# Performance work log

Measured on AMD Instinct MI355X. Metric: run time of the kernel, lower is better.

Reference implementation:

```python
import jax, jax.numpy as jnp
import numpy as np

N_USERS = 40000
N_ITEMS = 20000
NNZ = 1_000_000
D = 64
N_LAYERS = 3
EPS = 1e-8
PRUNING = 0.0  # forward default: pruning=0.0 -> get_sim_adj branch, threshold is a no-op


def setup_inputs() -> dict:
    key = jax.random.key(0)
    k1, k2, k3 = jax.random.split(key, 3)
    # unique-ish sorted edge codes -> coalesced COO order (sorted by (u, i))
    codes = jnp.sort(jax.random.randint(k3, (NNZ,), 0, N_USERS * N_ITEMS, dtype=jnp.int32))
    u_idx = codes // N_ITEMS
    i_idx = codes % N_ITEMS
    # xavier_uniform bound = sqrt(6/(fan_in+fan_out))
    b_u = float(np.sqrt(6.0 / (N_ITEMS + D)))
    b_i = float(np.sqrt(6.0 / (N_USERS + D)))
    user_linear = jax.random.uniform(k1, (N_ITEMS, D), jnp.float32, -b_u, b_u)
    item_linear = jax.random.uniform(k2, (N_USERS, D), jnp.float32, -b_i, b_i)
    return {"user_linear": user_linear, "item_linear": item_linear,
            "u_idx": u_idx, "i_idx": i_idx}


def reference(user_linear, item_linear, u_idx, i_idx):
    seg = jax.ops.segment_sum
    N = N_USERS + N_ITEMS
    # get_all_user_embedding: inter @ user_linear  -> [n_users, D]
    user_emb = seg(user_linear[i_idx], u_idx, num_segments=N_USERS)
    # get_all_item_embedding: inter.T @ item_linear -> [n_items, D]
    item_emb = seg(item_linear[u_idx], i_idx, num_segments=N_ITEMS)

    # sp_cos_sim: per-edge cosine similarity (chunked loop in torch == one vectorized gather)
    u_n = user_emb / jnp.maximum(jnp.linalg.norm(user_emb, axis=1, keepdims=True), EPS)
    i_n = item_emb / jnp.maximum(jnp.linalg.norm(item_emb, axis=1, keepdims=True), EPS)
    sims = jnp.sum(u_n[u_idx] * i_n[i_idx], axis=1)  # [nnz]
    # torch builds the sim sparse tensor with requires_grad=False -> detached
    sims = jax.lax.stop_gradient(sims)

    # inter2adj: values = [sims sorted by (u,i); sims sorted by (i,u)]
    sim_value = (sims + 1.0) * 0.5
    sim_value = jnp.where(sim_value < PRUNING, 0.0, sim_value) if PRUNING > 0 else sim_value
    perm = jnp.argsort(i_idx.astype(jnp.int32) * N_USERS + u_idx)  # (i,u) coalesce order
    rows = jnp.concatenate([u_idx, i_idx[perm] + N_USERS])          # [2*nnz]
    cols = jnp.concatenate([i_idx + N_USERS, u_idx[perm]])
    vals = jnp.concatenate([sim_value, sim_value[perm]])

    # row-normalize: D^-1 * A  (get_sim_adj)
    diags = seg(vals, rows, num_segments=N) + 1e-7
    vals = vals * (1.0 / diags)[rows]

    # LightGCN-style propagation
    all_emb = jnp.concatenate([user_emb, item_emb], axis=0)  # [N, D]
    embs = [all_emb]
    for _ in range(N_LAYERS):
        all_emb = seg(all_emb[cols] * vals[:, None], rows, num_segments=N)
        embs.append(all_emb)
    out = jnp.mean(jnp.stack(embs, axis=1), axis=1)  # [N, D]
    return out[:N_USERS], out[N_USERS:]
```

## Files before the change

kernel.cpp:

```cpp
#include <hip/hip_runtime.h>
#include <hip/hip_fp16.h>

#define N_USERS 40000
#define N_ITEMS 20000
#define N_TOTAL (N_USERS + N_ITEMS)
#define D 64
#define G_BKT ((N_ITEMS + 63) >> 6)
#define PAD 16

union H8 { uint4 u; __half h[8]; };

#define ZA (N_ITEMS * D / 8)
#define ZB (N_USERS * D / 8)
#define ZC (N_USERS + 1)
#define ZD ((G_BKT + 1) * PAD)
#define ZTOT (ZA + ZB + ZC + ZD)

__global__ void setup_kernel(const float* __restrict__ ul, const float* __restrict__ il,
                             const int* __restrict__ u_idx,
                             __half* __restrict__ ulH, __half* __restrict__ ilH,
                             int* __restrict__ pu, int* __restrict__ bcnt, int nnz) {
    int t = blockIdx.x * blockDim.x + threadIdx.x;
    if (t < ZA) {
        const float4* s = (const float4*)(ul + (size_t)t * 8);
        float4 a = s[0], b = s[1];
        H8 o;
        o.h[0] = __float2half(a.x); o.h[1] = __float2half(a.y);
        o.h[2] = __float2half(a.z); o.h[3] = __float2half(a.w);
        o.h[4] = __float2half(b.x); o.h[5] = __float2half(b.y);
        o.h[6] = __float2half(b.z); o.h[7] = __float2half(b.w);
        ((uint4*)ulH)[t] = o.u;
    } else if (t < ZA + ZB) {
        int q = t - ZA;
        const float4* s = (const float4*)(il + (size_t)q * 8);
        float4 a = s[0], b = s[1];
        H8 o;
        o.h[0] = __float2half(a.x); o.h[1] = __float2half(a.y);
        o.h[2] = __float2half(a.z); o.h[3] = __float2half(a.w);
        o.h[4] = __float2half(b.x); o.h[5] = __float2half(b.y);
        o.h[6] = __float2half(b.z); o.h[7] = __float2half(b.w);
        ((uint4*)ilH)[q] = o.u;
    } else if (t < ZA + ZB + ZC) {
        int u = t - (ZA + ZB);
        int lo = 0, hi = nnz;
        while (lo < hi) { int mid = (lo + hi) >> 1; if (u_idx[mid] < u) lo = mid + 1; else hi = mid; }
        pu[u] = lo;
    } else if (t < ZTOT) {
        bcnt[t - (ZA + ZB + ZC)] = 0;
    }
}


__global__ void bcount_kernel(const int* __restrict__ i_idx, int* __restrict__ bcnt, int nnz) {
    __shared__ int lc[G_BKT];
    for (int t = threadIdx.x; t < G_BKT; t += blockDim.x) lc[t] = 0;
    __syncthreads();
    int stride = gridDim.x * blockDim.x;
    for (int e = blockIdx.x * blockDim.x + threadIdx.x; e < nnz; e += stride)
        atomicAdd(&lc[__builtin_nontemporal_load(i_idx + e) >> 6], 1);
    __syncthreads();
    for (int t = threadIdx.x; t < G_BKT; t += blockDim.x)
        if (lc[t]) atomicAdd(bcnt + t * PAD, lc[t]);
}

__global__ void bscan_kernel(const int* __restrict__ bcnt, int* __restrict__ bbase,
                             int* __restrict__ bcur, int* __restrict__ pi, int nnz) {
    if (threadIdx.x == 0 && blockIdx.x == 0) {
        int run = 0;
        for (int g = 0; g < G_BKT; ++g) {
            bbase[g * PAD] = run;
            bcur[g * PAD] = run;
            run += bcnt[g * PAD];
        }
        bbase[G_BKT * PAD] = run;
        pi[N_ITEMS] = run;
    }
}

__global__ void p1_kernel(const int* __restrict__ i_idx, const int* __restrict__ u_idx,
                          int* __restrict__ bcur, int2* __restrict__ tmp, int nnz) {
    const int E = 8;
    __shared__ int lc[G_BKT];
    __shared__ int gb[G_BKT];
    for (int t = threadIdx.x; t < G_BKT; t += blockDim.x) lc[t] = 0;
    __syncthreads();
    int base_e = blockIdx.x * blockDim.x * E;
    int myb[E], myr[E]; int2 myv[E];
    #pragma unroll
    for (int j = 0; j < E; ++j) {
        int e = base_e + j * blockDim.x + threadIdx.x;
        myb[j] = -1;
        if (e < nnz) {
            int i = __builtin_nontemporal_load(i_idx + e);
            int u = __builtin_nontemporal_load(u_idx + e);
            int b = i >> 6;
            myb[j] = b;
            myr[j] = atomicAdd(&lc[b], 1);
            myv[j] = make_int2(e, (i << 16) | u);
        }
    }
    __syncthreads();
    for (int t = threadIdx.x; t < G_BKT; t += blockDim.x)
        gb[t] = lc[t] ? atomicAdd(bcur + t * PAD, lc[t]) : 0;
    __syncthreads();
    #pragma unroll
    for (int j = 0; j < E; ++j)
        if (myb[j] >= 0) tmp[gb[myb[j]] + myr[j]] = myv[j];
}

__global__ void p2_kernel(const int2* __restrict__ tmp, const int* __restrict__ bbase,
                          int* __restrict__ pi, int* __restrict__ eids, int* __restrict__ col2) {
    __shared__ int hist[64];
    __shared__ int cur[64];
    int g = blockIdx.x;
    int t = threadIdx.x;
    if (t < 64) { hist[t] = 0; cur[t] = 0; }
    __syncthreads();
    int base = bbase[g * PAD], end = bbase[(g + 1) * PAD];
    int lo_item = g << 6;
    for (int k = base + t; k < end; k += blockDim.x)
        atomicAdd(&hist[(tmp[k].y >> 16) & 63], 1);
    __syncthreads();
    if (t == 0) {
        int run = base;
        for (int x = 0; x < 64; ++x) {
            int c = hist[x];
            hist[x] = run;
            if (lo_item + x < N_ITEMS) pi[lo_item + x] = run;
            run += c;
        }
    }
    __syncthreads();
    for (int k = base + t; k < end; k += blockDim.x) {
        int2 v = tmp[k];
        int li = (v.y >> 16) & 63;
        int pos = atomicAdd(&cur[li], 1);
        int dst = hist[li] + pos;
        eids[dst] = v.x;
        col2[dst] = v.y & 0xFFFF;
    }
}

__global__ void diagw_kernel(const float* __restrict__ sims, const int* __restrict__ eids,
                             const int* __restrict__ pi, float* __restrict__ w2,
                             float* __restrict__ diag) {
    int i = (blockIdx.x * blockDim.x + threadIdx.x) >> 6;
    int lane = threadIdx.x & 63;
    if (i >= N_ITEMS) return;
    int b = pi[i], e = pi[i + 1];
    float s = 0.f;
    for (int k = b + lane; k < e; k += 64) {
        float w = sims[eids[k]];
        w2[k] = w;
        s += w;
    }
    #pragma unroll
    for (int m = 1; m < 64; m <<= 1) s += __shfl_xor(s, m, 64);
    if (lane == 0) diag[N_USERS + i] = s;
}

__global__ void emb_kernel(const __half* __restrict__ ulH, const __half* __restrict__ ilH,
                           const int* __restrict__ i_idx, const int* __restrict__ col2,
                           const int* __restrict__ pu, const int* __restrict__ pi,
                           __half* __restrict__ embH, float* __restrict__ invn) {
    int tid = blockIdx.x * blockDim.x + threadIdx.x;
    int wave = tid >> 6, lane = threadIdx.x & 63;
    int g = lane >> 3, c = lane & 7;
    int row = wave * 8 + g;
    if (row >= N_TOTAL) return;
    float s[8];
    #pragma unroll
    for (int j = 0; j < 8; ++j) s[j] = 0.f;
    const __half* tbl; const int* cols; int b, e;
    if (row < N_USERS) { tbl = ulH; cols = i_idx; b = pu[row]; e = pu[row + 1]; }
    else { int i = row - N_USERS; tbl = ilH; cols = col2; b = pi[i]; e = pi[i + 1]; }
    int k = b;
    for (; k + 3 < e; k += 4) {
        int i0 = cols[k], i1 = cols[k + 1], i2 = cols[k + 2], i3 = cols[k + 3];
        H8 r0, r1, r2, r3;
        r0.u = ((const uint4*)(tbl + (size_t)i0 * D))[c];
        r1.u = ((const uint4*)(tbl + (size_t)i1 * D))[c];
        r2.u = ((const uint4*)(tbl + (size_t)i2 * D))[c];
        r3.u = ((const uint4*)(tbl + (size_t)i3 * D))[c];
        #pragma unroll
        for (int q = 0; q < 8; ++q)
            s[q] += (__half2float(r0.h[q]) + __half2float(r1.h[q]))
                  + (__half2float(r2.h[q]) + __half2float(r3.h[q]));
    }
    for (; k < e; ++k) {
        H8 r0;
        r0.u = ((const uint4*)(tbl + (size_t)cols[k] * D))[c];
        #pragma unroll
        for (int q = 0; q < 8; ++q) s[q] += __half2float(r0.h[q]);
    }
    float nsq = 0.f;
    #pragma unroll
    for (int q = 0; q < 8; ++q) nsq += s[q] * s[q];
    #pragma unroll
    for (int m = 1; m < 8; m <<= 1) nsq += __shfl_xor(nsq, m, 64);
    H8 o;
    #pragma unroll
    for (int q = 0; q < 8; ++q) o.h[q] = __float2half(s[q]);
    ((uint4*)(embH + (size_t)row * D))[c] = o.u;
    if (c == 0) invn[row] = 1.f / fmaxf(sqrtf(nsq), 1e-8f);
}

__global__ void sims_kernel(const __half* __restrict__ embH, const float* __restrict__ invn,
                            const int* __restrict__ i_idx, const int* __restrict__ pu,
                            float* __restrict__ sims, float* __restrict__ diag) {
    int tid = blockIdx.x * blockDim.x + threadIdx.x;
    int wave = tid >> 6, lane = threadIdx.x & 63;
    int g = lane >> 3, c = lane & 7;
    int u = wave * 8 + g;
    if (u >= N_USERS) return;
    float invu = invn[u];
    H8 ur; ur.u = ((const uint4*)(embH + (size_t)u * D))[c];
    float un[8];
    #pragma unroll
    for (int j = 0; j < 8; ++j) un[j] = __half2float(ur.h[j]) * invu;
    int b = pu[u], e = pu[u + 1];
    float dsum = 0.f;
    int k = b;
    for (; k + 3 < e; k += 4) {
        int i0 = i_idx[k], i1 = i_idx[k + 1], i2 = i_idx[k + 2], i3 = i_idx[k + 3];
        H8 r0, r1, r2, r3;
        r0.u = ((const uint4*)(embH + (size_t)(N_USERS + i0) * D))[c];
        r1.u = ((const uint4*)(embH + (size_t)(N_USERS + i1) * D))[c];
        r2.u = ((const uint4*)(embH + (size_t)(N_USERS + i2) * D))[c];
        r3.u = ((const uint4*)(embH + (size_t)(N_USERS + i3) * D))[c];
        float d0 = 0.f, d1 = 0.f, d2 = 0.f, d3 = 0.f;
        #pragma unroll
        for (int q = 0; q < 8; ++q) {
            d0 += un[q] * __half2float(r0.h[q]);
            d1 += un[q] * __half2float(r1.h[q]);
            d2 += un[q] * __half2float(r2.h[q]);
            d3 += un[q] * __half2float(r3.h[q]);
        }
        #pragma unroll
        for (int m = 1; m < 8; m <<= 1) {
            d0 += __shfl_xor(d0, m, 64); d1 += __shfl_xor(d1, m, 64);
            d2 += __shfl_xor(d2, m, 64); d3 += __shfl_xor(d3, m, 64);
        }
        if (c == 0) {
            float sv0 = (d0 * invn[N_USERS + i0] + 1.f) * 0.5f;
            float sv1 = (d1 * invn[N_USERS + i1] + 1.f) * 0.5f;
            float sv2 = (d2 * invn[N_USERS + i2] + 1.f) * 0.5f;
            float sv3 = (d3 * invn[N_USERS + i3] + 1.f) * 0.5f;
            sims[k] = sv0; sims[k + 1] = sv1; sims[k + 2] = sv2; sims[k + 3] = sv3;
            dsum += (sv0 + sv1) + (sv2 + sv3);
        }
    }
    for (; k < e; ++k) {
        int i0 = i_idx[k];
        H8 r0;
        r0.u = ((const uint4*)(embH + (size_t)(N_USERS + i0) * D))[c];
        float d0 = 0.f;
        #pragma unroll
        for (int q = 0; q < 8; ++q) d0 += un[q] * __half2float(r0.h[q]);
        #pragma unroll
        for (int m = 1; m < 8; m <<= 1) d0 += __shfl_xor(d0, m, 64);
        if (c == 0) {
            float sv0 = (d0 * invn[N_USERS + i0] + 1.f) * 0.5f;
            sims[k] = sv0;
            dsum += sv0;
        }
    }
    if (c == 0) diag[u] = dsum;
}

template <bool FINAL>
__global__ void prop_kernel(const __half* __restrict__ curH, __half* __restrict__ nextH,
                            const float* __restrict__ sims, const float* __restrict__ w2,
                            const float* __restrict__ diag,
                            const int* __restrict__ i_idx, const int* __restrict__ col2,
                            const int* __restrict__ pu, const int* __restrict__ pi,
                            const __half* __restrict__ e0, const __half* __restrict__ e1,
                            const __half* __restrict__ e2, float* __restrict__ out) {
    int tid = blockIdx.x * blockDim.x + threadIdx.x;
    int wave = tid >> 6, lane = threadIdx.x & 63;
    int g = lane >> 3, c = lane & 7;
    int row = wave * 8 + g;
    if (row >= N_TOTAL) return;
    float s[8];
    #pragma unroll
    for (int j = 0; j < 8; ++j) s[j] = 0.f;
    const int* cols; const float* ws; int b, e, colOff;
    if (row < N_USERS) { b = pu[row]; e = pu[row + 1]; cols = i_idx; ws = sims; colOff = N_USERS; }
    else { int i = row - N_USERS; b = pi[i]; e = pi[i + 1]; cols = col2; ws = w2; colOff = 0; }
    int k = b;
    for (; k + 3 < e; k += 4) {
        int i0 = cols[k] + colOff, i1 = cols[k + 1] + colOff,
            i2 = cols[k + 2] + colOff, i3 = cols[k + 3] + colOff;
        float w0 = ws[k], w1 = ws[k + 1], w2v = ws[k + 2], w3v = ws[k + 3];
        H8 r0, r1, r2, r3;
        r0.u = ((const uint4*)(curH + (size_t)i0 * D))[c];
        r1.u = ((const uint4*)(curH + (size_t)i1 * D))[c];
        r2.u = ((const uint4*)(curH + (size_t)i2 * D))[c];
        r3.u = ((const uint4*)(curH + (size_t)i3 * D))[c];
        #pragma unroll
        for (int q = 0; q < 8; ++q)
            s[q] += (w0 * __half2float(r0.h[q]) + w1 * __half2float(r1.h[q]))
                  + (w2v * __half2float(r2.h[q]) + w3v * __half2float(r3.h[q]));
    }
    for (; k < e; ++k) {
        float w0 = ws[k];
        H8 r0;
        r0.u = ((const uint4*)(curH + (size_t)(cols[k] + colOff) * D))[c];
        #pragma unroll
        for (int q = 0; q < 8; ++q) s[q] += w0 * __half2float(r0.h[q]);
    }
    float invd = 1.f / (diag[row] + 1e-7f);
    float v[8];
    #pragma unroll
    for (int q = 0; q < 8; ++q) v[q] = s[q] * invd;
    if (FINAL) {
        H8 r0, r1, r2;
        r0.u = ((const uint4*)(e0 + (size_t)row * D))[c];
        r1.u = ((const uint4*)(e1 + (size_t)row * D))[c];
        r2.u = ((const uint4*)(e2 + (size_t)row * D))[c];
        float o[8];
        #pragma unroll
        for (int q = 0; q < 8; ++q)
            o[q] = (v[q] + __half2float(r0.h[q]) + __half2float(r1.h[q]) + __half2float(r2.h[q])) * 0.25f;
        float4* op = (float4*)(out + (size_t)row * D);
        op[c * 2]     = make_float4(o[0], o[1], o[2], o[3]);
        op[c * 2 + 1] = make_float4(o[4], o[5], o[6], o[7]);
    } else {
        H8 o;
        #pragma unroll
        for (int q = 0; q < 8; ++q) o.h[q] = __float2half(v[q]);
        ((uint4*)(nextH + (size_t)row * D))[c] = o.u;
    }
}


extern "C" void kernel_launch(void* const* d_in, const int* in_sizes, int n_in,
                              void* d_out, int out_size, void* d_ws, size_t ws_size,
                              hipStream_t stream) {
    const float* user_linear = (const float*)d_in[0];
    const float* item_linear = (const float*)d_in[1];
    const int* u_idx = (const int*)d_in[2];
    const int* i_idx = (const int*)d_in[3];
    const int nnz = in_sizes[2];

    char* p = (char*)d_ws;
    auto carve = [&](size_t bytes) { void* r = (void*)p; p += (bytes + 255) & ~(size_t)255; return r; };
    __half* embA = (__half*)carve((size_t)N_TOTAL * D * 2);
    __half* embB = (__half*)carve((size_t)N_TOTAL * D * 2);
    __half* embC = (__half*)carve((size_t)N_TOTAL * D * 2);
    __half* ulH  = (__half*)carve((size_t)N_ITEMS * D * 2);
    __half* ilH  = (__half*)carve((size_t)N_USERS * D * 2);
    float* sims = (float*)carve((size_t)nnz * 4);
    float* w2   = (float*)carve((size_t)nnz * 4);
    float* diag = (float*)carve((size_t)N_TOTAL * 4);
    float* invn = (float*)carve((size_t)N_TOTAL * 4);
    int* pu   = (int*)carve((size_t)(N_USERS + 1) * 4);
    int* pi   = (int*)carve((size_t)(N_ITEMS + 1) * 4);
    int* eids = (int*)carve((size_t)nnz * 4);
    int* col2 = (int*)carve((size_t)nnz * 4);
    int* bcnt  = (int*)carve((size_t)(G_BKT + 1) * PAD * 4);
    int* bbase = (int*)carve((size_t)(G_BKT + 1) * PAD * 4);
    int* bcur  = (int*)carve((size_t)(G_BKT + 1) * PAD * 4);

    int2* tmp = (int2*)embA;

    float* out = (float*)d_out;

    const int B = 256;

    setup_kernel<<<(ZTOT + B - 1) / B, B, 0, stream>>>(user_linear, item_linear, u_idx,
                                                       ulH, ilH, pu, bcnt, nnz);
    bcount_kernel<<<256, B, 0, stream>>>(i_idx, bcnt, nnz);
    bscan_kernel<<<1, 64, 0, stream>>>(bcnt, bbase, bcur, pi, nnz);
    p1_kernel<<<(nnz + B * 8 - 1) / (B * 8), B, 0, stream>>>(i_idx, u_idx, bcur, tmp, nnz);
    p2_kernel<<<G_BKT, B, 0, stream>>>(tmp, bbase, pi, eids, col2);

    int rowThreads = ((N_TOTAL + 7) / 8) * 64;
    emb_kernel<<<(rowThreads + B - 1) / B, B, 0, stream>>>(ulH, ilH, i_idx, col2,
                                                           pu, pi, embA, invn);

    int simThreads = ((N_USERS + 7) / 8) * 64;
    sims_kernel<<<(simThreads + B - 1) / B, B, 0, stream>>>(embA, invn, i_idx, pu, sims, diag);
    long long diThreads = (long long)N_ITEMS * 64;
    diagw_kernel<<<(int)((diThreads + B - 1) / B), B, 0, stream>>>(sims, eids, pi, w2, diag);

    prop_kernel<false><<<(rowThreads + B - 1) / B, B, 0, stream>>>(embA, embB, sims, w2, diag,
                                                                   i_idx, col2, pu, pi,
                                                                   nullptr, nullptr, nullptr, nullptr);
    prop_kernel<false><<<(rowThreads + B - 1) / B, B, 0, stream>>>(embB, embC, sims, w2, diag,
                                                                   i_idx, col2, pu, pi,
                                                                   nullptr, nullptr, nullptr, nullptr);
    prop_kernel<true><<<(rowThreads + B - 1) / B, B, 0, stream>>>(embC, nullptr, sims, w2, diag,
                                                                  i_idx, col2, pu, pi,
                                                                  embA, embB, embC, out);
}
```

Baseline: 238.8 us.

## Fuse cosine-sim, degree normalization and first propagation layer per row side

```diff
diff --git a/kernel.cpp b/kernel.cpp
--- a/kernel.cpp
+++ b/kernel.cpp
@@ -141,24 +141,6 @@
     }
 }
 
-__global__ void diagw_kernel(const float* __restrict__ sims, const int* __restrict__ eids,
-                             const int* __restrict__ pi, float* __restrict__ w2,
-                             float* __restrict__ diag) {
-    int i = (blockIdx.x * blockDim.x + threadIdx.x) >> 6;
-    int lane = threadIdx.x & 63;
-    if (i >= N_ITEMS) return;
-    int b = pi[i], e = pi[i + 1];
-    float s = 0.f;
-    for (int k = b + lane; k < e; k += 64) {
-        float w = sims[eids[k]];
-        w2[k] = w;
-        s += w;
-    }
-    #pragma unroll
-    for (int m = 1; m < 64; m <<= 1) s += __shfl_xor(s, m, 64);
-    if (lane == 0) diag[N_USERS + i] = s;
-}
-
 __global__ void emb_kernel(const __half* __restrict__ ulH, const __half* __restrict__ ilH,
                            const int* __restrict__ i_idx, const int* __restrict__ col2,
                            const int* __restrict__ pu, const int* __restrict__ pi,
@@ -205,29 +187,35 @@
     if (c == 0) invn[row] = 1.f / fmaxf(sqrtf(nsq), 1e-8f);
 }
 
-__global__ void sims_kernel(const __half* __restrict__ embH, const float* __restrict__ invn,
-                            const int* __restrict__ i_idx, const int* __restrict__ pu,
-                            float* __restrict__ sims, float* __restrict__ diag) {
+__global__ void fsp1u_kernel(const __half* __restrict__ embA, const float* __restrict__ invn,
+                             const int* __restrict__ i_idx, const int* __restrict__ pu,
+                             float* __restrict__ sims, float* __restrict__ diag,
+                             __half* __restrict__ embB) {
     int tid = blockIdx.x * blockDim.x + threadIdx.x;
     int wave = tid >> 6, lane = threadIdx.x & 63;
     int g = lane >> 3, c = lane & 7;
     int u = wave * 8 + g;
     if (u >= N_USERS) return;
     float invu = invn[u];
-    H8 ur; ur.u = ((const uint4*)(embH + (size_t)u * D))[c];
+    H8 ur; ur.u = ((const uint4*)(embA + (size_t)u * D))[c];
     float un[8];
     #pragma unroll
-    for (int j = 0; j < 8; ++j) un[j] = __half2float(ur.h[j]) * invu;
+    for (int q = 0; q < 8; ++q) un[q] = __half2float(ur.h[q]) * invu;
+    float s[8];
+    #pragma unroll
+    for (int q = 0; q < 8; ++q) s[q] = 0.f;
+    float dsum = 0.f;
     int b = pu[u], e = pu[u + 1];
-    float dsum = 0.f;
     int k = b;
     for (; k + 3 < e; k += 4) {
         int i0 = i_idx[k], i1 = i_idx[k + 1], i2 = i_idx[k + 2], i3 = i_idx[k + 3];
         H8 r0, r1, r2, r3;
-        r0.u = ((const uint4*)(embH + (size_t)(N_USERS + i0) * D))[c];
-        r1.u = ((const uint4*)(embH + (size_t)(N_USERS + i1) * D))[c];
-        r2.u = ((const uint4*)(embH + (size_t)(N_USERS + i2) * D))[c];
-        r3.u = ((const uint4*)(embH + (size_t)(N_USERS + i3) * D))[c];
+        r0.u = ((const uint4*)(embA + (size_t)(N_USERS + i0) * D))[c];
+        r1.u = ((const uint4*)(embA + (size_t)(N_USERS + i1) * D))[c];
+        r2.u = ((const uint4*)(embA + (size_t)(N_USERS + i2) * D))[c];
+        r3.u = ((const uint4*)(embA + (size_t)(N_USERS + i3) * D))[c];
+        float iv0 = invn[N_USERS + i0], iv1 = invn[N_USERS + i1];
+        float iv2 = invn[N_USERS + i2], iv3 = invn[N_USERS + i3];
         float d0 = 0.f, d1 = 0.f, d2 = 0.f, d3 = 0.f;
         #pragma unroll
         for (int q = 0; q < 8; ++q) {
@@ -241,31 +229,87 @@
             d0 += __shfl_xor(d0, m, 64); d1 += __shfl_xor(d1, m, 64);
             d2 += __shfl_xor(d2, m, 64); d3 += __shfl_xor(d3, m, 64);
         }
-        if (c == 0) {
-            float sv0 = (d0 * invn[N_USERS + i0] + 1.f) * 0.5f;
-            float sv1 = (d1 * invn[N_USERS + i1] + 1.f) * 0.5f;
-            float sv2 = (d2 * invn[N_USERS + i2] + 1.f) * 0.5f;
-            float sv3 = (d3 * invn[N_USERS + i3] + 1.f) * 0.5f;
-            sims[k] = sv0; sims[k + 1] = sv1; sims[k + 2] = sv2; sims[k + 3] = sv3;
-            dsum += (sv0 + sv1) + (sv2 + sv3);
-        }
+        float sv0 = (d0 * iv0 + 1.f) * 0.5f;
+        float sv1 = (d1 * iv1 + 1.f) * 0.5f;
+        float sv2 = (d2 * iv2 + 1.f) * 0.5f;
+        float sv3 = (d3 * iv3 + 1.f) * 0.5f;
+        if (c == 0) { sims[k] = sv0; sims[k + 1] = sv1; sims[k + 2] = sv2; sims[k + 3] = sv3; }
+        dsum += (sv0 + sv1) + (sv2 + sv3);
+        #pragma unroll
+        for (int q = 0; q < 8; ++q)
+            s[q] += (sv0 * __half2float(r0.h[q]) + sv1 * __half2float(r1.h[q]))
+                  + (sv2 * __half2float(r2.h[q]) + sv3 * __half2float(r3.h[q]));
     }
     for (; k < e; ++k) {
         int i0 = i_idx[k];
         H8 r0;
-        r0.u = ((const uint4*)(embH + (size_t)(N_USERS + i0) * D))[c];
+        r0.u = ((const uint4*)(embA + (size_t)(N_USERS + i0) * D))[c];
+        float iv0 = invn[N_USERS + i0];
         float d0 = 0.f;
         #pragma unroll
         for (int q = 0; q < 8; ++q) d0 += un[q] * __half2float(r0.h[q]);
         #pragma unroll
         for (int m = 1; m < 8; m <<= 1) d0 += __shfl_xor(d0, m, 64);
-        if (c == 0) {
-            float sv0 = (d0 * invn[N_USERS + i0] + 1.f) * 0.5f;
-            sims[k] = sv0;
-            dsum += sv0;
-        }
+        float sv0 = (d0 * iv0 + 1.f) * 0.5f;
+        if (c == 0) sims[k] = sv0;
+        dsum += sv0;
+        #pragma unroll
+        for (int q = 0; q < 8; ++q) s[q] += sv0 * __half2float(r0.h[q]);
     }
     if (c == 0) diag[u] = dsum;
+    float invd = 1.f / (dsum + 1e-7f);
+    H8 o;
+    #pragma unroll
+    for (int q = 0; q < 8; ++q) o.h[q] = __float2half(s[q] * invd);
+    ((uint4*)(embB + (size_t)u * D))[c] = o.u;
+}
+
+__global__ void p1i_kernel(const __half* __restrict__ embA, const float* __restrict__ sims,
+                           const int* __restrict__ eids, const int* __restrict__ col2,
+                           const int* __restrict__ pi, float* __restrict__ w2,
+                           float* __restrict__ diag, __half* __restrict__ embB) {
+    int tid = blockIdx.x * blockDim.x + threadIdx.x;
+    int wave = tid >> 6, lane = threadIdx.x & 63;
+    int g = lane >> 3, c = lane & 7;
+    int i = wave * 8 + g;
+    if (i >= N_ITEMS) return;
+    float s[8];
+    #pragma unroll
+    for (int q = 0; q < 8; ++q) s[q] = 0.f;
+    float dsum = 0.f;
+    int b = pi[i], e = pi[i + 1];
+    int k = b;
+    for (; k + 3 < e; k += 4) {
+        int e0 = eids[k], e1 = eids[k + 1], e2 = eids[k + 2], e3 = eids[k + 3];
+        int u0 = col2[k], u1 = col2[k + 1], u2 = col2[k + 2], u3 = col2[k + 3];
+        float w0 = sims[e0], w1 = sims[e1], w2v = sims[e2], w3v = sims[e3];
+        H8 r0, r1, r2, r3;
+        r0.u = ((const uint4*)(embA + (size_t)u0 * D))[c];
+        r1.u = ((const uint4*)(embA + (size_t)u1 * D))[c];
+        r2.u = ((const uint4*)(embA + (size_t)u2 * D))[c];
+        r3.u = ((const uint4*)(embA + (size_t)u3 * D))[c];
+        if (c == 0) { w2[k] = w0; w2[k + 1] = w1; w2[k + 2] = w2v; w2[k + 3] = w3v; }
+        dsum += (w0 + w1) + (w2v + w3v);
+        #pragma unroll
+        for (int q = 0; q < 8; ++q)
+            s[q] += (w0 * __half2float(r0.h[q]) + w1 * __half2float(r1.h[q]))
+                  + (w2v * __half2float(r2.h[q]) + w3v * __half2float(r3.h[q]));
+    }
+    for (; k < e; ++k) {
+        float w0 = sims[eids[k]];
+        H8 r0;
+        r0.u = ((const uint4*)(embA + (size_t)col2[k] * D))[c];
+        if (c == 0) w2[k] = w0;
+        dsum += w0;
+        #pragma unroll
+        for (int q = 0; q < 8; ++q) s[q] += w0 * __half2float(r0.h[q]);
+    }
+    if (c == 0) diag[N_USERS + i] = dsum;
+    float invd = 1.f / (dsum + 1e-7f);
+    H8 o;
+    #pragma unroll
+    for (int q = 0; q < 8; ++q) o.h[q] = __float2half(s[q] * invd);
+    ((uint4*)(embB + (size_t)(N_USERS + i) * D))[c] = o.u;
 }
 
 template <bool FINAL>
@@ -379,14 +423,13 @@
     emb_kernel<<<(rowThreads + B - 1) / B, B, 0, stream>>>(ulH, ilH, i_idx, col2,
                                                            pu, pi, embA, invn);
 
-    int simThreads = ((N_USERS + 7) / 8) * 64;
-    sims_kernel<<<(simThreads + B - 1) / B, B, 0, stream>>>(embA, invn, i_idx, pu, sims, diag);
-    long long diThreads = (long long)N_ITEMS * 64;
-    diagw_kernel<<<(int)((diThreads + B - 1) / B), B, 0, stream>>>(sims, eids, pi, w2, diag);
-
-    prop_kernel<false><<<(rowThreads + B - 1) / B, B, 0, stream>>>(embA, embB, sims, w2, diag,
-                                                                   i_idx, col2, pu, pi,
-                                                                   nullptr, nullptr, nullptr, nullptr);
+    int uThreads = ((N_USERS + 7) / 8) * 64;
+    fsp1u_kernel<<<(uThreads + B - 1) / B, B, 0, stream>>>(embA, invn, i_idx, pu,
+                                                           sims, diag, embB);
+    int iThreads = ((N_ITEMS + 7) / 8) * 64;
+    p1i_kernel<<<(iThreads + B - 1) / B, B, 0, stream>>>(embA, sims, eids, col2, pi,
+                                                         w2, diag, embB);
+
     prop_kernel<false><<<(rowThreads + B - 1) / B, B, 0, stream>>>(embB, embC, sims, w2, diag,
                                                                    i_idx, col2, pu, pi,
                                                                    nullptr, nullptr, nullptr, nullptr);
```

Measured after the change: 232.8 us (median of 2 runs). -2.5%, faster.
